# Kernel optimization log

Hardware: AMD Instinct MI355X
Metric: run time of the kernel (lower is better)

Reference implementation:

```python
import jax, jax.numpy as jnp
import numpy as np

DIM = 256
NH = 8
PD = DIM // 16  # DynamicPosBias pos_dim = (dim//4)//4 = 16
B_ = 256
GH = 16
GW = 16
N = GH * GW
NG = 64


def setup_inputs() -> dict:
    key = jax.random.key(0)
    ks = jax.random.split(key, 24)
    s = 0.05
    inp = {
        "q": jax.random.normal(ks[0], (B_, N, DIM), dtype=jnp.float32),
        "k": jax.random.normal(ks[1], (B_, N, DIM), dtype=jnp.float32),
        "mask": jax.random.normal(ks[2], (NG, N, N), dtype=jnp.float32),
        "q_w": jax.random.normal(ks[3], (DIM, DIM), dtype=jnp.float32) * s,
        "q_b": jnp.zeros((DIM,), jnp.float32),
        "kv_w": jax.random.normal(ks[4], (2 * DIM, DIM), dtype=jnp.float32) * s,
        "kv_b": jnp.zeros((2 * DIM,), jnp.float32),
        "proj_w": jax.random.normal(ks[5], (DIM, DIM), dtype=jnp.float32) * s,
        "proj_b": jnp.zeros((DIM,), jnp.float32),
        "pp_w": jax.random.normal(ks[6], (PD, 2), dtype=jnp.float32) * s,
        "pp_b": jnp.zeros((PD,), jnp.float32),
        "ln1_g": jnp.ones((PD,), jnp.float32),
        "ln1_b": jnp.zeros((PD,), jnp.float32),
        "l1_w": jax.random.normal(ks[7], (PD, PD), dtype=jnp.float32) * s,
        "l1_b": jnp.zeros((PD,), jnp.float32),
        "ln2_g": jnp.ones((PD,), jnp.float32),
        "ln2_b": jnp.zeros((PD,), jnp.float32),
        "l2_w": jax.random.normal(ks[8], (PD, PD), dtype=jnp.float32) * s,
        "l2_b": jnp.zeros((PD,), jnp.float32),
        "ln3_g": jnp.ones((PD,), jnp.float32),
        "ln3_b": jnp.zeros((PD,), jnp.float32),
        "l3_w": jax.random.normal(ks[9], (NH, PD), dtype=jnp.float32) * s,
        "l3_b": jnp.zeros((NH,), jnp.float32),
        "H": GH,
        "W": GW,
    }
    return inp


def _ln(x, g, b):
    m = x.mean(-1, keepdims=True)
    v = ((x - m) ** 2).mean(-1, keepdims=True)
    return (x - m) / jnp.sqrt(v + 1e-5) * g + b


def _pos_bias(H, W, pp_w, pp_b, ln1_g, ln1_b, l1_w, l1_b, ln2_g, ln2_b, l2_w, l2_b, ln3_g, ln3_b, l3_w, l3_b):
    # biases: ((2H-1)*(2W-1), 2) relative offsets
    bh = jnp.arange(1 - H, H, dtype=jnp.float32)
    bw = jnp.arange(1 - W, W, dtype=jnp.float32)
    mg = jnp.stack(jnp.meshgrid(bh, bw, indexing="ij"))  # (2, 2H-1, 2W-1)
    biases = mg.reshape(2, -1).T  # (L, 2)
    # MLP (residual=False): pos3(pos2(pos1(pos_proj(b))))
    x = biases @ pp_w.T + pp_b
    x = _ln(x, ln1_g, ln1_b)
    x = jax.nn.relu(x) @ l1_w.T + l1_b
    x = _ln(x, ln2_g, ln2_b)
    x = jax.nn.relu(x) @ l2_w.T + l2_b
    x = _ln(x, ln3_g, ln3_b)
    pos = jax.nn.relu(x) @ l3_w.T + l3_b  # (L, NH)
    # relative position index (N, N)
    ch = jnp.arange(H)
    cw = jnp.arange(W)
    coords = jnp.stack(jnp.meshgrid(ch, cw, indexing="ij")).reshape(2, -1)  # (2, N)
    rel = coords[:, :, None] - coords[:, None, :]  # (2, N, N)
    rel = rel.transpose(1, 2, 0)
    rel = rel + jnp.array([H - 1, W - 1])
    idx = rel[..., 0] * (2 * W - 1) + rel[..., 1]  # (N, N)
    rpb = pos[idx.reshape(-1)].reshape(H * W, H * W, -1)  # (N, N, NH)
    return rpb.transpose(2, 0, 1)  # (NH, N, N)


def reference(q, k, mask, q_w, q_b, kv_w, kv_b, proj_w, proj_b, pp_w, pp_b,
              ln1_g, ln1_b, l1_w, l1_b, ln2_g, ln2_b, l2_w, l2_b,
              ln3_g, ln3_b, l3_w, l3_b, H, W):
    B, n, C = q.shape
    hd = C // NH
    scale = hd ** -0.5
    qh = (q @ q_w.T + q_b).reshape(B, n, NH, hd).transpose(0, 2, 1, 3)  # (B, NH, N, hd)
    kvh = (k @ kv_w.T + kv_b).reshape(B, n, 2, NH, hd).transpose(2, 0, 3, 1, 4)
    kh, vh = kvh[0], kvh[1]
    attn = jnp.einsum("bhnd,bhmd->bhnm", qh * scale, kh)
    rpb = _pos_bias(H, W, pp_w, pp_b, ln1_g, ln1_b, l1_w, l1_b,
                    ln2_g, ln2_b, l2_w, l2_b, ln3_g, ln3_b, l3_w, l3_b)
    attn = attn + rpb[None]
    nG = mask.shape[0]
    attn = attn.reshape(B // nG, nG, NH, n, n) + mask[None, :, None]
    attn = jax.nn.softmax(attn.reshape(B, NH, n, n), axis=-1)
    x = jnp.einsum("bhnm,bhmd->bhnd", attn, vh).transpose(0, 2, 1, 3).reshape(B, n, C)
    return x @ proj_w.T + proj_b
```

## Files before the change

### kernel.cpp

```cpp
#include <hip/hip_runtime.h>
#include <hip/hip_bf16.h>
#include <cstdint>
#include <cstddef>

typedef __bf16 bf16x8 __attribute__((ext_vector_type(8)));
typedef __bf16 bf16x4 __attribute__((ext_vector_type(4)));
typedef float floatx4 __attribute__((ext_vector_type(4)));

__device__ __forceinline__ floatx4 mfma16x16x32(bf16x8 a, bf16x8 b, floatx4 c) {
    return __builtin_amdgcn_mfma_f32_16x16x32_bf16(a, b, c, 0, 0, 0);
}

__device__ __forceinline__ bool flag_is_f32(const void* ones) {
    return *(const unsigned int*)ones == 0x3F800000u;
}
__device__ __forceinline__ float ld1(const void* p, int i, bool f32) {
    return f32 ? ((const float*)p)[i] : (float)((const __bf16*)p)[i];
}
__device__ __forceinline__ bf16x8 ld8(const void* p, size_t i, bool f32) {
    if (f32) {
        const float* f = (const float*)p + i;
        float4 a = *(const float4*)f;
        float4 b = *(const float4*)(f + 4);
        bf16x8 v;
        v[0] = (__bf16)a.x; v[1] = (__bf16)a.y; v[2] = (__bf16)a.z; v[3] = (__bf16)a.w;
        v[4] = (__bf16)b.x; v[5] = (__bf16)b.y; v[6] = (__bf16)b.z; v[7] = (__bf16)b.w;
        return v;
    }
    return *(const bf16x8*)((const __bf16*)p + i);
}

__device__ __forceinline__ void ln16(float* x, const void* g, const void* b, bool f32) {
    float m = 0.f;
    for (int j = 0; j < 16; ++j) m += x[j];
    m *= (1.f / 16.f);
    float v = 0.f;
    for (int j = 0; j < 16; ++j) { float d = x[j] - m; v += d * d; }
    v *= (1.f / 16.f);
    float inv = rsqrtf(v + 1e-5f);
    for (int j = 0; j < 16; ++j)
        x[j] = (x[j] - m) * inv * ld1(g, j, f32) + ld1(b, j, f32);
}

__global__ void __launch_bounds__(256) k_rpbT(
    const void* __restrict__ pp_w, const void* __restrict__ pp_b,
    const void* __restrict__ g1, const void* __restrict__ b1,
    const void* __restrict__ w1, const void* __restrict__ c1,
    const void* __restrict__ g2, const void* __restrict__ b2,
    const void* __restrict__ w2, const void* __restrict__ c2,
    const void* __restrict__ g3, const void* __restrict__ b3,
    const void* __restrict__ w3, const void* __restrict__ c3,
    __bf16* __restrict__ rpbT)
{
    const bool f32 = flag_is_f32(g1);
    const int bid = blockIdx.x;
    const int j = bid & 255, h = bid >> 8;
    const int i = threadIdx.x;
    const int dy = (i >> 4) - (j >> 4) + 15;
    const int dx = (i & 15) - (j & 15) + 15;
    const float by = (float)(dy - 15), bx = (float)(dx - 15);

    float x[16], y[16];
    for (int o = 0; o < 16; ++o)
        x[o] = by * ld1(pp_w, 2 * o, f32) + bx * ld1(pp_w, 2 * o + 1, f32) + ld1(pp_b, o, f32);
    ln16(x, g1, b1, f32);
    for (int o = 0; o < 16; ++o) {
        float s = ld1(c1, o, f32);
        for (int jj = 0; jj < 16; ++jj) s += fmaxf(x[jj], 0.f) * ld1(w1, o * 16 + jj, f32);
        y[o] = s;
    }
    ln16(y, g2, b2, f32);
    for (int o = 0; o < 16; ++o) {
        float s = ld1(c2, o, f32);
        for (int jj = 0; jj < 16; ++jj) s += fmaxf(y[jj], 0.f) * ld1(w2, o * 16 + jj, f32);
        x[o] = s;
    }
    ln16(x, g3, b3, f32);
    float s = ld1(c3, h, f32);
    for (int jj = 0; jj < 16; ++jj) s += fmaxf(x[jj], 0.f) * ld1(w3, h * 16 + jj, f32);
    rpbT[(size_t)h * 65536 + (size_t)j * 256 + i] = (__bf16)s;
}

__global__ void __launch_bounds__(256) k_maskT(const void* __restrict__ mask,
                                               __bf16* __restrict__ maskT,
                                               const void* __restrict__ flag)
{
    __shared__ float sT[64][65];
    const bool f32 = flag_is_f32(flag);
    const int g = blockIdx.x;
    const int tl = blockIdx.y;
    const int i0 = (tl & 3) * 64, j0 = (tl >> 2) * 64;
    const size_t gbase = (size_t)g * 65536;
    __bf16* mo = maskT + gbase;
    const int t = threadIdx.x;
    for (int n = 0; n < 16; ++n) {
        int e = n * 256 + t;
        int r = e >> 6, c = e & 63;
        sT[r][c] = ld1(mask, (int)(gbase + (size_t)(i0 + r) * 256 + j0 + c), f32);
    }
    __syncthreads();
    for (int n = 0; n < 16; ++n) {
        int e = n * 256 + t;
        int jj = e >> 6, ii = e & 63;
        mo[(size_t)(j0 + jj) * 256 + i0 + ii] = (__bf16)sT[ii][jj];
    }
}

template <int MODE>
__global__ void __launch_bounds__(256) k_gemm(
    const void* __restrict__ A, const void* __restrict__ W,
    const void* __restrict__ bias, void* __restrict__ out0,
    __bf16* __restrict__ out1, const void* __restrict__ flag)
{
    __shared__ __bf16 sA[128 * 40];
    __shared__ __bf16 sB[128 * 40];
    const bool in_f32 = flag_is_f32(flag);
    const bool af32 = (MODE == 2) ? false : in_f32;
    const int m0 = blockIdx.x * 128;
    const int n0 = blockIdx.y * 128;
    const int t = threadIdx.x;
    const int w = t >> 6;
    const int lane = t & 63;
    const int lm = lane & 15, q = lane >> 4;

    floatx4 acc[2][8];
    for (int a_ = 0; a_ < 2; ++a_)
        for (int b_ = 0; b_ < 8; ++b_)
            for (int r = 0; r < 4; ++r) acc[a_][b_][r] = 0.f;

    for (int kc = 0; kc < 256; kc += 32) {
        for (int s = 0; s < 2; ++s) {
            int u = t + s * 256;
            int row = u >> 2, seg = u & 3;
            *(bf16x8*)&sA[row * 40 + seg * 8] =
                ld8(A, (size_t)(m0 + row) * 256 + kc + seg * 8, af32);
            *(bf16x8*)&sB[row * 40 + seg * 8] =
                ld8(W, (size_t)(n0 + row) * 256 + kc + seg * 8, in_f32);
        }
        __syncthreads();
        bf16x8 af[2], bfr[8];
        for (int rt = 0; rt < 2; ++rt)
            af[rt] = *(const bf16x8*)&sA[(w * 32 + rt * 16 + lm) * 40 + q * 8];
        for (int ct = 0; ct < 8; ++ct)
            bfr[ct] = *(const bf16x8*)&sB[(ct * 16 + lm) * 40 + q * 8];
        for (int rt = 0; rt < 2; ++rt)
            for (int ct = 0; ct < 8; ++ct)
                acc[rt][ct] = mfma16x16x32(af[rt], bfr[ct], acc[rt][ct]);
        __syncthreads();
    }

    for (int rt = 0; rt < 2; ++rt) {
        const int rbase = m0 + w * 32 + rt * 16 + q * 4;
        for (int ct = 0; ct < 8; ++ct) {
            const int gc = n0 + ct * 16 + lm;
            const float bv = ld1(bias, gc, in_f32);
            for (int r = 0; r < 4; ++r) {
                const int gr = rbase + r;
                float v = acc[rt][ct][r] + bv;
                if (MODE == 0) {
                    int b = gr >> 8, nn = gr & 255, h = gc >> 5, d = gc & 31;
                    ((__bf16*)out0)[(((size_t)(b * 8 + h)) * 256 + nn) * 32 + d] =
                        (__bf16)(v * 0.17677669529663687f);
                } else if (MODE == 1) {
                    int b = gr >> 8, nn = gr & 255;
                    int f = gc & 255, h = f >> 5, d = f & 31;
                    __bf16* dst = (gc < 256) ? (__bf16*)out0 : out1;
                    dst[(((size_t)(b * 8 + h)) * 256 + nn) * 32 + d] = (__bf16)v;
                } else {
                    if (in_f32) ((float*)out0)[(size_t)gr * 256 + gc] = v;
                    else        ((__bf16*)out0)[(size_t)gr * 256 + gc] = (__bf16)v;
                }
            }
        }
    }
}

__global__ void __launch_bounds__(256) k_attn(
    const __bf16* __restrict__ qs, const __bf16* __restrict__ ks,
    const __bf16* __restrict__ vs, const __bf16* __restrict__ maskT,
    const __bf16* __restrict__ rpbT, __bf16* __restrict__ xb)
{
    __shared__ __bf16 sK[256 * 36];
    __shared__ __bf16 sV[32 * 264];
    __shared__ __bf16 sP[4 * 16 * 136];
    const int bid = blockIdx.x;
    const int x = bid & 7, rr = bid >> 3;
    const int g = x + ((rr & 7) << 3);
    const int h = (rr >> 3) & 7;
    const int bi = rr >> 6;
    const int b = g + (bi << 6);
    const int t = threadIdx.x, w = t >> 6, lane = t & 63;
    const int lm = lane & 15, q = lane >> 4;
    const size_t bh = (size_t)(b * 8 + h);
    const __bf16* qb = qs + bh * 8192;
    const __bf16* kb = ks + bh * 8192;
    const __bf16* vb = vs + bh * 8192;
    const __bf16* mT = maskT + (size_t)g * 65536;
    const __bf16* rT = rpbT + (size_t)h * 65536;

    for (int s = 0; s < 4; ++s) {
        int u = t + s * 256;
        int row = u >> 2, seg = u & 3;
        *(bf16x8*)&sK[row * 36 + seg * 8] = *(const bf16x8*)&kb[row * 32 + seg * 8];
    }
    {
        bf16x8 vr[4];
        for (int s = 0; s < 4; ++s)
            vr[s] = *(const bf16x8*)&vb[t * 32 + s * 8];
        for (int s = 0; s < 4; ++s)
            for (int j = 0; j < 8; ++j)
                sV[(s * 8 + j) * 264 + t] = vr[s][j];
    }
    __syncthreads();

    __bf16* sPw = sP + w * (16 * 136);
    for (int rt = 0; rt < 4; ++rt) {
        const int row16 = w * 64 + rt * 16;
        const bf16x8 aq = *(const bf16x8*)&qb[(size_t)(row16 + lm) * 32 + q * 8];

        floatx4 acc[16];
        for (int ct = 0; ct < 16; ++ct)
            for (int r = 0; r < 4; ++r) acc[ct][r] = 0.f;
        for (int ct = 0; ct < 16; ++ct) {
            const bf16x8 bk = *(const bf16x8*)&sK[(ct * 16 + lm) * 36 + q * 8];
            acc[ct] = mfma16x16x32(aq, bk, acc[ct]);
        }
        for (int ct = 0; ct < 16; ++ct) {
            const int col = ct * 16 + lm;
            const bf16x4 mv = *(const bf16x4*)&mT[(size_t)col * 256 + row16 + q * 4];
            const bf16x4 rv = *(const bf16x4*)&rT[(size_t)col * 256 + row16 + q * 4];
            for (int r = 0; r < 4; ++r)
                acc[ct][r] += (float)mv[r] + (float)rv[r];
        }
        float mx[4], inv[4];
        for (int r = 0; r < 4; ++r) {
            float m = acc[0][r];
            for (int ct = 1; ct < 16; ++ct) m = fmaxf(m, acc[ct][r]);
            for (int d = 1; d < 16; d <<= 1) m = fmaxf(m, __shfl_xor(m, d));
            mx[r] = m;
        }
        for (int r = 0; r < 4; ++r) {
            float s = 0.f;
            for (int ct = 0; ct < 16; ++ct) {
                float p = __expf(acc[ct][r] - mx[r]);
                acc[ct][r] = p;
                s += p;
            }
            for (int d = 1; d < 16; d <<= 1) s += __shfl_xor(s, d);
            inv[r] = 1.f / s;
        }
        floatx4 o0, o1;
        for (int r = 0; r < 4; ++r) { o0[r] = 0.f; o1[r] = 0.f; }
        for (int half = 0; half < 2; ++half) {
            __syncthreads();
            for (int ct = 0; ct < 8; ++ct) {
                const int c = half * 8 + ct;
                for (int r = 0; r < 4; ++r)
                    sPw[(q * 4 + r) * 136 + ct * 16 + lm] = (__bf16)acc[c][r];
            }
            __syncthreads();
            for (int ksl = 0; ksl < 4; ++ksl) {
                const bf16x8 ap = *(const bf16x8*)&sPw[lm * 136 + ksl * 32 + q * 8];
                const bf16x8 bv0 =
                    *(const bf16x8*)&sV[lm * 264 + half * 128 + ksl * 32 + q * 8];
                const bf16x8 bv1 =
                    *(const bf16x8*)&sV[(16 + lm) * 264 + half * 128 + ksl * 32 + q * 8];
                o0 = mfma16x16x32(ap, bv0, o0);
                o1 = mfma16x16x32(ap, bv1, o1);
            }
        }
        for (int r = 0; r < 4; ++r) {
            const size_t row = (size_t)b * 256 + row16 + q * 4 + r;
            xb[row * 256 + h * 32 + lm]      = (__bf16)(o0[r] * inv[r]);
            xb[row * 256 + h * 32 + 16 + lm] = (__bf16)(o1[r] * inv[r]);
        }
    }
}

extern "C" void kernel_launch(void* const* d_in, const int* in_sizes, int n_in,
                              void* d_out, int out_size, void* d_ws, size_t ws_size,
                              hipStream_t stream)
{
    const void* q      = d_in[0];
    const void* k      = d_in[1];
    const void* mask   = d_in[2];
    const void* q_w    = d_in[3];
    const void* q_b    = d_in[4];
    const void* kv_w   = d_in[5];
    const void* kv_b   = d_in[6];
    const void* proj_w = d_in[7];
    const void* proj_b = d_in[8];
    const void* flag   = d_in[11];

    char* ws = (char*)d_ws;
    __bf16* qs    = (__bf16*)(ws);
    __bf16* ksb   = (__bf16*)(ws + (size_t)33554432);
    __bf16* vsb   = (__bf16*)(ws + (size_t)2 * 33554432);
    __bf16* xbuf  = (__bf16*)(ws + (size_t)3 * 33554432);
    __bf16* maskT = (__bf16*)(ws + (size_t)4 * 33554432);
    __bf16* rpbT  = (__bf16*)(ws + (size_t)4 * 33554432 + 8388608);

    k_rpbT<<<2048, 256, 0, stream>>>(
        d_in[9],  d_in[10], d_in[11], d_in[12], d_in[13], d_in[14],
        d_in[15], d_in[16], d_in[17], d_in[18], d_in[19], d_in[20],
        d_in[21], d_in[22], rpbT);
    k_maskT<<<dim3(64, 16), 256, 0, stream>>>(mask, maskT, flag);
    k_gemm<0><<<dim3(512, 2), 256, 0, stream>>>(q, q_w, q_b, qs, nullptr, flag);
    k_gemm<1><<<dim3(512, 4), 256, 0, stream>>>(k, kv_w, kv_b, ksb, vsb, flag);
    k_attn<<<2048, 256, 0, stream>>>(qs, ksb, vsb, maskT, rpbT, xbuf);
    k_gemm<2><<<dim3(512, 2), 256, 0, stream>>>(xbuf, proj_w, proj_b, d_out, nullptr, flag);
}
```

Baseline: 587.3 us.

## Compute transposed scores to keep P in registers and drop mask transpose

```diff
diff --git a/kernel.cpp b/kernel.cpp
--- a/kernel.cpp
+++ b/kernel.cpp
@@ -6,6 +6,7 @@
 typedef __bf16 bf16x8 __attribute__((ext_vector_type(8)));
 typedef __bf16 bf16x4 __attribute__((ext_vector_type(4)));
 typedef float floatx4 __attribute__((ext_vector_type(4)));
+typedef unsigned int uint32x4 __attribute__((ext_vector_type(4)));
 
 __device__ __forceinline__ floatx4 mfma16x16x32(bf16x8 a, bf16x8 b, floatx4 c) {
     return __builtin_amdgcn_mfma_f32_16x16x32_bf16(a, b, c, 0, 0, 0);
@@ -28,6 +29,12 @@
         return v;
     }
     return *(const bf16x8*)((const __bf16*)p + i);
+}
+__device__ __forceinline__ unsigned int pk2(float a, float b) {
+    __bf16 x = (__bf16)a, y = (__bf16)b;
+    unsigned short ux = __builtin_bit_cast(unsigned short, x);
+    unsigned short uy = __builtin_bit_cast(unsigned short, y);
+    return (unsigned int)ux | ((unsigned int)uy << 16);
 }
 
 __device__ __forceinline__ void ln16(float* x, const void* g, const void* b, bool f32) {
@@ -50,14 +57,14 @@
     const void* __restrict__ w2, const void* __restrict__ c2,
     const void* __restrict__ g3, const void* __restrict__ b3,
     const void* __restrict__ w3, const void* __restrict__ c3,
-    __bf16* __restrict__ rpbT)
+    __bf16* __restrict__ rpbD)
 {
     const bool f32 = flag_is_f32(g1);
     const int bid = blockIdx.x;
-    const int j = bid & 255, h = bid >> 8;
-    const int i = threadIdx.x;
-    const int dy = (i >> 4) - (j >> 4) + 15;
-    const int dx = (i & 15) - (j & 15) + 15;
+    const int ii = bid & 255, h = bid >> 8;
+    const int jj = threadIdx.x;
+    const int dy = (ii >> 4) - (jj >> 4) + 15;
+    const int dx = (ii & 15) - (jj & 15) + 15;
     const float by = (float)(dy - 15), bx = (float)(dx - 15);
 
     float x[16], y[16];
@@ -66,44 +73,29 @@
     ln16(x, g1, b1, f32);
     for (int o = 0; o < 16; ++o) {
         float s = ld1(c1, o, f32);
-        for (int jj = 0; jj < 16; ++jj) s += fmaxf(x[jj], 0.f) * ld1(w1, o * 16 + jj, f32);
+        for (int k = 0; k < 16; ++k) s += fmaxf(x[k], 0.f) * ld1(w1, o * 16 + k, f32);
         y[o] = s;
     }
     ln16(y, g2, b2, f32);
     for (int o = 0; o < 16; ++o) {
         float s = ld1(c2, o, f32);
-        for (int jj = 0; jj < 16; ++jj) s += fmaxf(y[jj], 0.f) * ld1(w2, o * 16 + jj, f32);
+        for (int k = 0; k < 16; ++k) s += fmaxf(y[k], 0.f) * ld1(w2, o * 16 + k, f32);
         x[o] = s;
     }
     ln16(x, g3, b3, f32);
     float s = ld1(c3, h, f32);
-    for (int jj = 0; jj < 16; ++jj) s += fmaxf(x[jj], 0.f) * ld1(w3, h * 16 + jj, f32);
-    rpbT[(size_t)h * 65536 + (size_t)j * 256 + i] = (__bf16)s;
-}
-
-__global__ void __launch_bounds__(256) k_maskT(const void* __restrict__ mask,
-                                               __bf16* __restrict__ maskT,
+    for (int k = 0; k < 16; ++k) s += fmaxf(x[k], 0.f) * ld1(w3, h * 16 + k, f32);
+    rpbD[(size_t)h * 65536 + (size_t)ii * 256 + jj] = (__bf16)s;
+}
+
+__global__ void __launch_bounds__(256) k_maskC(const void* __restrict__ mask,
+                                               __bf16* __restrict__ maskD,
                                                const void* __restrict__ flag)
 {
-    __shared__ float sT[64][65];
     const bool f32 = flag_is_f32(flag);
-    const int g = blockIdx.x;
-    const int tl = blockIdx.y;
-    const int i0 = (tl & 3) * 64, j0 = (tl >> 2) * 64;
-    const size_t gbase = (size_t)g * 65536;
-    __bf16* mo = maskT + gbase;
-    const int t = threadIdx.x;
-    for (int n = 0; n < 16; ++n) {
-        int e = n * 256 + t;
-        int r = e >> 6, c = e & 63;
-        sT[r][c] = ld1(mask, (int)(gbase + (size_t)(i0 + r) * 256 + j0 + c), f32);
-    }
-    __syncthreads();
-    for (int n = 0; n < 16; ++n) {
-        int e = n * 256 + t;
-        int jj = e >> 6, ii = e & 63;
-        mo[(size_t)(j0 + jj) * 256 + i0 + ii] = (__bf16)sT[ii][jj];
-    }
+    const size_t i = ((size_t)blockIdx.x * 256 + threadIdx.x) * 8;
+    bf16x8 v = ld8(mask, i, f32);
+    *(bf16x8*)&maskD[i] = v;
 }
 
 template <int MODE>
@@ -175,14 +167,13 @@
     }
 }
 
-__global__ void __launch_bounds__(256) k_attn(
+__global__ void __launch_bounds__(256, 4) k_attn(
     const __bf16* __restrict__ qs, const __bf16* __restrict__ ks,
-    const __bf16* __restrict__ vs, const __bf16* __restrict__ maskT,
-    const __bf16* __restrict__ rpbT, __bf16* __restrict__ xb)
+    const __bf16* __restrict__ vs, const __bf16* __restrict__ maskD,
+    const __bf16* __restrict__ rpbD, __bf16* __restrict__ xb)
 {
     __shared__ __bf16 sK[256 * 36];
-    __shared__ __bf16 sV[32 * 264];
-    __shared__ __bf16 sP[4 * 16 * 136];
+    __shared__ __bf16 sV[32 * 266];
     const int bid = blockIdx.x;
     const int x = bid & 7, rr = bid >> 3;
     const int g = x + ((rr & 7) << 3);
@@ -195,9 +186,10 @@
     const __bf16* qb = qs + bh * 8192;
     const __bf16* kb = ks + bh * 8192;
     const __bf16* vb = vs + bh * 8192;
-    const __bf16* mT = maskT + (size_t)g * 65536;
-    const __bf16* rT = rpbT + (size_t)h * 65536;
-
+    const __bf16* mD = maskD + (size_t)g * 65536;
+    const __bf16* rD = rpbD + (size_t)h * 65536;
+
+#pragma unroll
     for (int s = 0; s < 4; ++s) {
         int u = t + s * 256;
         int row = u >> 2, seg = u & 3;
@@ -205,74 +197,91 @@
     }
     {
         bf16x8 vr[4];
+#pragma unroll
         for (int s = 0; s < 4; ++s)
             vr[s] = *(const bf16x8*)&vb[t * 32 + s * 8];
+#pragma unroll
         for (int s = 0; s < 4; ++s)
+#pragma unroll
             for (int j = 0; j < 8; ++j)
-                sV[(s * 8 + j) * 264 + t] = vr[s][j];
+                sV[(s * 8 + j) * 266 + t] = vr[s][j];
     }
     __syncthreads();
 
-    __bf16* sPw = sP + w * (16 * 136);
     for (int rt = 0; rt < 4; ++rt) {
         const int row16 = w * 64 + rt * 16;
         const bf16x8 aq = *(const bf16x8*)&qb[(size_t)(row16 + lm) * 32 + q * 8];
 
         floatx4 acc[16];
+#pragma unroll
         for (int ct = 0; ct < 16; ++ct)
             for (int r = 0; r < 4; ++r) acc[ct][r] = 0.f;
+        __builtin_amdgcn_s_setprio(1);
+#pragma unroll
         for (int ct = 0; ct < 16; ++ct) {
             const bf16x8 bk = *(const bf16x8*)&sK[(ct * 16 + lm) * 36 + q * 8];
-            acc[ct] = mfma16x16x32(aq, bk, acc[ct]);
-        }
+            acc[ct] = mfma16x16x32(bk, aq, acc[ct]);
+        }
+        __builtin_amdgcn_s_setprio(0);
+        const size_t brow = (size_t)(row16 + lm) * 256 + q * 4;
+#pragma unroll
         for (int ct = 0; ct < 16; ++ct) {
-            const int col = ct * 16 + lm;
-            const bf16x4 mv = *(const bf16x4*)&mT[(size_t)col * 256 + row16 + q * 4];
-            const bf16x4 rv = *(const bf16x4*)&rT[(size_t)col * 256 + row16 + q * 4];
+            const bf16x4 mv = *(const bf16x4*)&mD[brow + ct * 16];
+            const bf16x4 rv = *(const bf16x4*)&rD[brow + ct * 16];
+#pragma unroll
             for (int r = 0; r < 4; ++r)
                 acc[ct][r] += (float)mv[r] + (float)rv[r];
         }
-        float mx[4], inv[4];
+        float m = acc[0][0];
+#pragma unroll
+        for (int ct = 0; ct < 16; ++ct)
+            for (int r = 0; r < 4; ++r) m = fmaxf(m, acc[ct][r]);
+        m = fmaxf(m, __shfl_xor(m, 16));
+        m = fmaxf(m, __shfl_xor(m, 32));
+        float ssum = 0.f;
+#pragma unroll
+        for (int ct = 0; ct < 16; ++ct)
+            for (int r = 0; r < 4; ++r) {
+                float p = __expf(acc[ct][r] - m);
+                acc[ct][r] = p;
+                ssum += p;
+            }
+        ssum += __shfl_xor(ssum, 16);
+        ssum += __shfl_xor(ssum, 32);
+        const float inv = 1.f / ssum;
+        unsigned int pk[16][2];
+#pragma unroll
+        for (int ct = 0; ct < 16; ++ct) {
+            pk[ct][0] = pk2(acc[ct][0], acc[ct][1]);
+            pk[ct][1] = pk2(acc[ct][2], acc[ct][3]);
+        }
+        floatx4 o0, o1;
+#pragma unroll
+        for (int r = 0; r < 4; ++r) { o0[r] = 0.f; o1[r] = 0.f; }
+#pragma unroll
+        for (int ct2 = 0; ct2 < 8; ++ct2) {
+            uint32x4 dw;
+#pragma unroll
+            for (int i = 0; i < 4; ++i) {
+                const int srcl = ((q & 1) * 2 + (i >> 1)) * 16 + lm;
+                const int ta = __shfl((int)pk[2 * ct2][i & 1], srcl);
+                const int tb = __shfl((int)pk[2 * ct2 + 1][i & 1], srcl);
+                dw[i] = (q >> 1) ? (unsigned int)tb : (unsigned int)ta;
+            }
+            const bf16x8 ap = __builtin_bit_cast(bf16x8, dw);
+            const bf16x8 bv0 = *(const bf16x8*)&sV[lm * 266 + ct2 * 32 + q * 8];
+            const bf16x8 bv1 = *(const bf16x8*)&sV[(16 + lm) * 266 + ct2 * 32 + q * 8];
+            __builtin_amdgcn_s_setprio(1);
+            o0 = mfma16x16x32(ap, bv0, o0);
+            o1 = mfma16x16x32(ap, bv1, o1);
+            __builtin_amdgcn_s_setprio(0);
+        }
+#pragma unroll
         for (int r = 0; r < 4; ++r) {
-            float m = acc[0][r];
-            for (int ct = 1; ct < 16; ++ct) m = fmaxf(m, acc[ct][r]);
-            for (int d = 1; d < 16; d <<= 1) m = fmaxf(m, __shfl_xor(m, d));
-            mx[r] = m;
-        }
-        for (int r = 0; r < 4; ++r) {
-            float s = 0.f;
-            for (int ct = 0; ct < 16; ++ct) {
-                float p = __expf(acc[ct][r] - mx[r]);
-                acc[ct][r] = p;
-                s += p;
-            }
-            for (int d = 1; d < 16; d <<= 1) s += __shfl_xor(s, d);
-            inv[r] = 1.f / s;
-        }
-        floatx4 o0, o1;
-        for (int r = 0; r < 4; ++r) { o0[r] = 0.f; o1[r] = 0.f; }
-        for (int half = 0; half < 2; ++half) {
-            __syncthreads();
-            for (int ct = 0; ct < 8; ++ct) {
-                const int c = half * 8 + ct;
-                for (int r = 0; r < 4; ++r)
-                    sPw[(q * 4 + r) * 136 + ct * 16 + lm] = (__bf16)acc[c][r];
-            }
-            __syncthreads();
-            for (int ksl = 0; ksl < 4; ++ksl) {
-                const bf16x8 ap = *(const bf16x8*)&sPw[lm * 136 + ksl * 32 + q * 8];
-                const bf16x8 bv0 =
-                    *(const bf16x8*)&sV[lm * 264 + half * 128 + ksl * 32 + q * 8];
-                const bf16x8 bv1 =
-                    *(const bf16x8*)&sV[(16 + lm) * 264 + half * 128 + ksl * 32 + q * 8];
-                o0 = mfma16x16x32(ap, bv0, o0);
-                o1 = mfma16x16x32(ap, bv1, o1);
-            }
-        }
-        for (int r = 0; r < 4; ++r) {
+            const float invr = __shfl(inv, (lane & 48) + ((lane >> 4) << 2) + r);
             const size_t row = (size_t)b * 256 + row16 + q * 4 + r;
-            xb[row * 256 + h * 32 + lm]      = (__bf16)(o0[r] * inv[r]);
-            xb[row * 256 + h * 32 + 16 + lm] = (__bf16)(o1[r] * inv[r]);
+            xb[row * 256 + h * 32 + lm]      = (__bf16)(o0[r] * invr);
+            xb[row * 256 + h * 32 + 16 + lm] = (__bf16)(o1[r] * invr);
         }
     }
 }
@@ -297,16 +306,16 @@
     __bf16* ksb   = (__bf16*)(ws + (size_t)33554432);
     __bf16* vsb   = (__bf16*)(ws + (size_t)2 * 33554432);
     __bf16* xbuf  = (__bf16*)(ws + (size_t)3 * 33554432);
-    __bf16* maskT = (__bf16*)(ws + (size_t)4 * 33554432);
-    __bf16* rpbT  = (__bf16*)(ws + (size_t)4 * 33554432 + 8388608);
+    __bf16* maskD = (__bf16*)(ws + (size_t)4 * 33554432);
+    __bf16* rpbD  = (__bf16*)(ws + (size_t)4 * 33554432 + 8388608);
 
     k_rpbT<<<2048, 256, 0, stream>>>(
         d_in[9],  d_in[10], d_in[11], d_in[12], d_in[13], d_in[14],
         d_in[15], d_in[16], d_in[17], d_in[18], d_in[19], d_in[20],
-        d_in[21], d_in[22], rpbT);
-    k_maskT<<<dim3(64, 16), 256, 0, stream>>>(mask, maskT, flag);
+        d_in[21], d_in[22], rpbD);
+    k_maskC<<<2048, 256, 0, stream>>>(mask, maskD, flag);
     k_gemm<0><<<dim3(512, 2), 256, 0, stream>>>(q, q_w, q_b, qs, nullptr, flag);
     k_gemm<1><<<dim3(512, 4), 256, 0, stream>>>(k, kv_w, kv_b, ksb, vsb, flag);
-    k_attn<<<2048, 256, 0, stream>>>(qs, ksb, vsb, maskT, rpbT, xbuf);
+    k_attn<<<2048, 256, 0, stream>>>(qs, ksb, vsb, maskD, rpbD, xbuf);
     k_gemm<2><<<dim3(512, 2), 256, 0, stream>>>(xbuf, proj_w, proj_b, d_out, nullptr, flag);
 }
```

New measurement: 699.8 us. +19.2%, slower.
